# Kernel optimization log

Measured on AMD Instinct MI355X. Metric: run time of the kernel, lower is better.

The kernel has to match this reference:

```python
import jax, jax.numpy as jnp
import numpy as np

NUM_BITS = 10
MEM_SIZE = 2 ** NUM_BITS  # 1024
HIDDEN = 1024
INPUT = 1024
BATCH = 16384
LN_EPS = 1e-5


def setup_inputs() -> dict:
    key = jax.random.key(0)
    ks = jax.random.split(key, 8)
    s = 0.02
    return {
        "x": jax.random.normal(ks[0], (BATCH, INPUT), jnp.float32),
        "h_prev": jax.random.normal(ks[1], (BATCH, HIDDEN), jnp.float32),
        "memory": jax.random.normal(ks[2], (MEM_SIZE, HIDDEN), jnp.float32),
        "W_w": jax.random.normal(ks[3], (HIDDEN, INPUT), jnp.float32) * s,
        "W_b": jnp.zeros((HIDDEN,), jnp.float32),
        "U_w": jax.random.normal(ks[4], (HIDDEN, HIDDEN), jnp.float32) * s,
        "U_b": jnp.zeros((HIDDEN,), jnp.float32),
        "Q_w": jax.random.normal(ks[5], (HIDDEN, HIDDEN), jnp.float32) * s,
        "Q_b": jnp.zeros((HIDDEN,), jnp.float32),
        "M_w": jax.random.normal(ks[6], (NUM_BITS, HIDDEN), jnp.float32) * s,
        "M_b": jnp.zeros((NUM_BITS,), jnp.float32),
        "ln_g": jnp.ones((HIDDEN,), jnp.float32),
        "ln_b": jnp.zeros((HIDDEN,), jnp.float32),
    }


def reference(x, h_prev, memory, W_w, W_b, U_w, U_b, Q_w, Q_b, M_w, M_b, ln_g, ln_b):
    # Binary address from h_prev (eval-mode hard threshold, non-differentiable)
    powers = jnp.asarray(2 ** np.arange(NUM_BITS - 1, -1, -1), dtype=x.dtype)  # [num_bits]
    logits = h_prev @ M_w.T + M_b                              # [B, num_bits]
    binary = (jax.nn.sigmoid(logits) > 0.5).astype(x.dtype)    # hard bits
    index = jnp.clip((binary * powers).sum(-1).astype(jnp.int32), 0, MEM_SIZE - 1)  # [B]
    h_mem = memory[index]                                      # gather [B, H]
    # Fused linear combine + LayerNorm + sigmoid
    pre = x @ W_w.T + W_b + h_prev @ U_w.T + U_b + h_mem @ Q_w.T + Q_b  # [B, H]
    mu = pre.mean(-1, keepdims=True)
    var = ((pre - mu) ** 2).mean(-1, keepdims=True)            # biased var (torch LN)
    norm = (pre - mu) * jax.lax.rsqrt(var + LN_EPS)
    return jax.nn.sigmoid(norm * ln_g + ln_b)                  # h_new [B, H]
```

## Files before the change

### kernel.cpp

```cpp
#include <hip/hip_runtime.h>

#define BATCH   16384
#define HIDDEN  1024
#define K2      2048
#define MEMSZ   1024
#define NBITS   10

#define BM 256
#define BN 256
#define BK 64
#define NT (K2 / BK)

typedef __bf16 bf16x8 __attribute__((ext_vector_type(8)));
typedef float  f32x4  __attribute__((ext_vector_type(4)));

__device__ __forceinline__ unsigned short f2bf(float f) {
    unsigned int u = __float_as_uint(f);
    u += 0x7FFFu + ((u >> 16) & 1u);
    return (unsigned short)(u >> 16);
}

__device__ __forceinline__ void gload_lds16(const void* g, void* l) {
    __builtin_amdgcn_global_load_lds(
        (const __attribute__((address_space(1))) unsigned int*)g,
        (__attribute__((address_space(3))) unsigned int*)l,
        16, 0, 0);
}

__global__ void pack_kernel(const float* __restrict__ W,
                            const float* __restrict__ U,
                            const float* __restrict__ memory,
                            const float* __restrict__ Q,
                            unsigned short* __restrict__ Bm,
                            unsigned short* __restrict__ Mem,
                            unsigned short* __restrict__ Qb) {
    int u = blockIdx.x * 256 + threadIdx.x;
    const float* src;
    unsigned short* dst;
    if (u < 524288) {
        int n = u >> 9;
        int k = (u & 511) * 4;
        src = (k < 1024) ? (W + (size_t)n * 1024 + k)
                         : (U + (size_t)n * 1024 + (k - 1024));
        dst = Bm + (size_t)n * K2 + k;
    } else if (u < 786432) {
        int f = (u - 524288) * 4;
        src = memory + f;  dst = Mem + f;
    } else if (u < 1048576) {
        int f = (u - 786432) * 4;
        src = Q + f;  dst = Qb + f;
    } else return;
    float4 v = *reinterpret_cast<const float4*>(src);
    ushort4 o;
    o.x = f2bf(v.x); o.y = f2bf(v.y); o.z = f2bf(v.z); o.w = f2bf(v.w);
    *reinterpret_cast<ushort4*>(dst) = o;
}

__global__ __launch_bounds__(256) void mq_kernel(
        const unsigned short* __restrict__ Mem,
        const unsigned short* __restrict__ Qb,
        float* __restrict__ MQ) {
    __shared__ unsigned short As[128 * 64];
    __shared__ unsigned short Bs[128 * 64];

    const int ks = blockIdx.x >> 6;
    const int mb = (blockIdx.x >> 3) & 7;
    const int nb = blockIdx.x & 7;
    const int t    = threadIdx.x;
    const int lane = t & 63;
    const int w    = t >> 6;
    const int wr   = w >> 1, wc = w & 1;
    const int rr   = lane & 15, rq = lane >> 4;
    const int c8   = (t & 7) * 8;
    const int srow = t >> 3;

    f32x4 acc[4][4] = {};

    for (int kt = 0; kt < 4; ++kt) {
        const int k0 = ks * 256 + kt * 64;
#pragma unroll
        for (int i = 0; i < 4; ++i) {
            int r = i * 32 + srow;
            gload_lds16(Mem + (size_t)(mb * 128 + r) * 1024 + k0 + c8, As + i * 2048 + t * 8);
            gload_lds16(Qb  + (size_t)(nb * 128 + r) * 1024 + k0 + c8, Bs + i * 2048 + t * 8);
        }
        __syncthreads();
#pragma unroll
        for (int kk = 0; kk < 2; ++kk) {
            const int krd = kk * 32 + rq * 8;
            bf16x8 af[4], bfv[4];
#pragma unroll
            for (int m = 0; m < 4; ++m)
                af[m] = *reinterpret_cast<const bf16x8*>(As + (wr * 64 + m * 16 + rr) * 64 + krd);
#pragma unroll
            for (int n = 0; n < 4; ++n)
                bfv[n] = *reinterpret_cast<const bf16x8*>(Bs + (wc * 64 + n * 16 + rr) * 64 + krd);
#pragma unroll
            for (int m = 0; m < 4; ++m)
#pragma unroll
                for (int n = 0; n < 4; ++n)
                    acc[m][n] = __builtin_amdgcn_mfma_f32_16x16x32_bf16(
                        af[m], bfv[n], acc[m][n], 0, 0, 0);
        }
        __syncthreads();
    }

#pragma unroll
    for (int m = 0; m < 4; ++m)
#pragma unroll
        for (int n = 0; n < 4; ++n) {
            int gcol = nb * 128 + wc * 64 + n * 16 + rr;
#pragma unroll
            for (int j = 0; j < 4; ++j) {
                int grow = mb * 128 + wr * 64 + m * 16 + rq * 4 + j;
                atomicAdd(&MQ[(size_t)grow * 1024 + gcol], acc[m][n][j]);
            }
        }
}

__global__ __launch_bounds__(256) void build_a_kernel(
        const float* __restrict__ x,
        const float* __restrict__ h_prev,
        const float* __restrict__ M_w,
        const float* __restrict__ M_b,
        unsigned short* __restrict__ A,
        int* __restrict__ idxbuf) {
    int row  = (blockIdx.x * blockDim.x + threadIdx.x) >> 6;
    int lane = threadIdx.x & 63;
    if (row >= BATCH) return;

    const float4* hp = reinterpret_cast<const float4*>(h_prev + (size_t)row * HIDDEN);
    float4 hv[4];
#pragma unroll
    for (int i = 0; i < 4; ++i) hv[i] = hp[i * 64 + lane];

    int idx = 0;
#pragma unroll
    for (int j = 0; j < NBITS; ++j) {
        const float4* mp = reinterpret_cast<const float4*>(M_w + (size_t)j * HIDDEN);
        float s = 0.f;
#pragma unroll
        for (int i = 0; i < 4; ++i) {
            float4 m = mp[i * 64 + lane];
            s += hv[i].x * m.x + hv[i].y * m.y + hv[i].z * m.z + hv[i].w * m.w;
        }
#pragma unroll
        for (int off = 32; off >= 1; off >>= 1) s += __shfl_xor(s, off, 64);
        float logit = s + M_b[j];
        if (logit > 0.f) idx |= (1 << (NBITS - 1 - j));
    }
    if (lane == 0) idxbuf[row] = idx;

    unsigned short* arow = A + (size_t)row * K2;
    const float4* xp = reinterpret_cast<const float4*>(x + (size_t)row * HIDDEN);
#pragma unroll
    for (int i = 0; i < 4; ++i) {
        int off = i * 256 + lane * 4;
        float4 vx = xp[i * 64 + lane];
        ushort4 ox; ox.x = f2bf(vx.x); ox.y = f2bf(vx.y); ox.z = f2bf(vx.z); ox.w = f2bf(vx.w);
        *reinterpret_cast<ushort4*>(arow + off) = ox;

        ushort4 oh; oh.x = f2bf(hv[i].x); oh.y = f2bf(hv[i].y); oh.z = f2bf(hv[i].z); oh.w = f2bf(hv[i].w);
        *reinterpret_cast<ushort4*>(arow + 1024 + off) = oh;
    }
}


__device__ __forceinline__ void stage_g(const unsigned short* __restrict__ src,
                                        int rowbase, int kt, int g,
                                        unsigned short* ldsTile, int t) {
    const int o      = g * 8192 + t * 16;
    const int row    = o >> 7;
    const int inner  = o & 127;
    const int sinner = inner ^ ((row & 7) << 4);
    const char* gp = reinterpret_cast<const char*>(
                         src + (size_t)(rowbase + row) * K2 + kt * BK) + sinner;
    gload_lds16(gp, reinterpret_cast<char*>(ldsTile) + o);
}

__device__ __forceinline__ bf16x8 ldsfrag(const unsigned short* tile, int row,
                                          int kbyte_x_sw) {
    return *reinterpret_cast<const bf16x8*>(
        reinterpret_cast<const char*>(tile) + row * 128 + kbyte_x_sw);
}

#define BAR_IN()                                                     \
    do {                                                             \
        asm volatile("" ::: "memory");                               \
        __builtin_amdgcn_s_barrier();                                \
        asm volatile("s_waitcnt lgkmcnt(0)" ::: "memory");           \
        __builtin_amdgcn_sched_barrier(0);                           \
    } while (0)

#define BAR_OUT()                                                    \
    do {                                                             \
        __builtin_amdgcn_sched_barrier(0);                           \
        asm volatile("" ::: "memory");                               \
        __builtin_amdgcn_s_barrier();                                \
    } while (0)

#define MFMA_Q(MB, NB)                                                         \
    {                                                                          \
        __builtin_amdgcn_s_setprio(1);                                         \
        _Pragma("unroll") for (int m_ = 0; m_ < 4; ++m_)                       \
        _Pragma("unroll") for (int n_ = 0; n_ < 2; ++n_)                       \
        _Pragma("unroll") for (int kk_ = 0; kk_ < 2; ++kk_)                    \
            acc[(MB) + m_][(NB) + n_] =                                        \
                __builtin_amdgcn_mfma_f32_16x16x32_bf16(                       \
                    af[m_][kk_], bfr[(NB) + n_][kk_],                          \
                    acc[(MB) + m_][(NB) + n_], 0, 0, 0);                       \
        __builtin_amdgcn_s_setprio(0);                                         \
    }

__global__ __launch_bounds__(512, 2) void gemm_kernel(
        const unsigned short* __restrict__ A,
        const unsigned short* __restrict__ Bm,
        float* __restrict__ C) {
    __shared__ alignas(16) unsigned short lds[2][2][BM * BK];

    const int bid  = blockIdx.x;
    const int wgid = (bid & 7) * 32 + (bid >> 3);
    const int mblk = wgid >> 2;
    const int nblk = wgid & 3;

    const int t    = threadIdx.x;
    const int lane = t & 63;
    const int w    = t >> 6;
    const int wr   = w >> 2;
    const int wc   = w & 3;
    const int rr   = lane & 15;
    const int rq   = lane >> 4;
    const int sw   = (rr & 7) << 4;
    const int rqb  = rq * 16;
    const int wrb  = wr * 128;
    const int wcb  = wc * 64;

    const int arow = mblk * BM;
    const int brow = nblk * BN;

    f32x4 acc[8][4] = {};

    {
#pragma unroll
        for (int g = 0; g < 4; ++g) stage_g(A,  arow, 0, g, &lds[0][0][0], t);
#pragma unroll
        for (int g = 0; g < 4; ++g) stage_g(Bm, brow, 0, g, &lds[0][1][0], t);
#pragma unroll
        for (int g = 0; g < 4; ++g) stage_g(Bm, brow, 1, g, &lds[1][1][0], t);
#pragma unroll
        for (int g = 0; g < 2; ++g) stage_g(A,  arow, 1, g, &lds[1][0][0], t);
        asm volatile("s_waitcnt vmcnt(6)" ::: "memory");
        asm volatile("" ::: "memory");
        __builtin_amdgcn_s_barrier();
    }

    bf16x8 af[4][2];
    bf16x8 bfr[4][2];

#pragma unroll 2
    for (int kt = 0; kt < NT; ++kt) {
        const int c = kt & 1;
        const unsigned short* At = &lds[c][0][0];
        const unsigned short* Bt = &lds[c][1][0];
        unsigned short* nxA  = &lds[c ^ 1][0][0];
        unsigned short* curA = &lds[c][0][0];
        unsigned short* curB = &lds[c][1][0];

#pragma unroll
        for (int m = 0; m < 4; ++m) {
            af[m][0] = ldsfrag(At, wrb + m * 16 + rr, (rqb) ^ sw);
            af[m][1] = ldsfrag(At, wrb + m * 16 + rr, (64 + rqb) ^ sw);
        }
#pragma unroll
        for (int n = 0; n < 4; ++n) {
            bfr[n][0] = ldsfrag(Bt, wcb + n * 16 + rr, (rqb) ^ sw);
            bfr[n][1] = ldsfrag(Bt, wcb + n * 16 + rr, (64 + rqb) ^ sw);
        }
        if (kt + 1 < NT) {
            stage_g(A, arow, kt + 1, 2, nxA, t);
            stage_g(A, arow, kt + 1, 3, nxA, t);
        }
        BAR_IN();
        MFMA_Q(0, 0);
        BAR_OUT();

        BAR_IN();
        MFMA_Q(0, 2);
        BAR_OUT();

#pragma unroll
        for (int m = 0; m < 4; ++m) {
            af[m][0] = ldsfrag(At, wrb + 64 + m * 16 + rr, (rqb) ^ sw);
            af[m][1] = ldsfrag(At, wrb + 64 + m * 16 + rr, (64 + rqb) ^ sw);
        }
        if (kt + 2 < NT) {
            stage_g(Bm, brow, kt + 2, 0, curB, t);
            stage_g(Bm, brow, kt + 2, 1, curB, t);
        }
        BAR_IN();
        MFMA_Q(4, 0);
        BAR_OUT();

        if (kt + 2 < NT) {
            stage_g(Bm, brow, kt + 2, 2, curB, t);
            stage_g(Bm, brow, kt + 2, 3, curB, t);
            stage_g(A,  arow, kt + 2, 0, curA, t);
            stage_g(A,  arow, kt + 2, 1, curA, t);
        }
        BAR_IN();
        MFMA_Q(4, 2);
        __builtin_amdgcn_sched_barrier(0);
        if (kt < NT - 2) {
            asm volatile("s_waitcnt vmcnt(6)" ::: "memory");
        } else if (kt == NT - 2) {
            asm volatile("s_waitcnt vmcnt(0)" ::: "memory");
        }
        asm volatile("" ::: "memory");
        __builtin_amdgcn_s_barrier();
    }

#pragma unroll
    for (int mi = 0; mi < 8; ++mi) {
#pragma unroll
        for (int n = 0; n < 4; ++n) {
            const int gcol = nblk * BN + wcb + n * 16 + rr;
#pragma unroll
            for (int j = 0; j < 4; ++j) {
                const int grow = mblk * BM + wrb + mi * 16 + rq * 4 + j;
                C[(size_t)grow * HIDDEN + gcol] = acc[mi][n][j];
            }
        }
    }
}

__global__ __launch_bounds__(256) void ln_kernel(
        float* __restrict__ C,
        const int* __restrict__ idxbuf,
        const float* __restrict__ MQ,
        const float* __restrict__ W_b, const float* __restrict__ U_b,
        const float* __restrict__ Q_b, const float* __restrict__ ln_g,
        const float* __restrict__ ln_b) {
    const int row = blockIdx.x;
    const int t   = threadIdx.x;
    const int midx = idxbuf[row];
    float4* rowp = reinterpret_cast<float4*>(C + (size_t)row * HIDDEN);
    const float4* mqp = reinterpret_cast<const float4*>(MQ + (size_t)midx * HIDDEN);

    float4 p  = rowp[t];
    float4 mq = mqp[t];
    float4 bw = reinterpret_cast<const float4*>(W_b)[t];
    float4 bu = reinterpret_cast<const float4*>(U_b)[t];
    float4 bq = reinterpret_cast<const float4*>(Q_b)[t];
    p.x += mq.x + bw.x + bu.x + bq.x;
    p.y += mq.y + bw.y + bu.y + bq.y;
    p.z += mq.z + bw.z + bu.z + bq.z;
    p.w += mq.w + bw.w + bu.w + bq.w;

    float s  = p.x + p.y + p.z + p.w;
    float sq = p.x * p.x + p.y * p.y + p.z * p.z + p.w * p.w;
#pragma unroll
    for (int off = 32; off >= 1; off >>= 1) {
        s  += __shfl_xor(s,  off, 64);
        sq += __shfl_xor(sq, off, 64);
    }
    __shared__ float red[8];
    const int lane = t & 63, w = t >> 6;
    if (lane == 0) { red[w] = s; red[4 + w] = sq; }
    __syncthreads();
    const float S    = red[0] + red[1] + red[2] + red[3];
    const float SQ   = red[4] + red[5] + red[6] + red[7];
    const float mean = S * (1.0f / HIDDEN);
    const float var  = SQ * (1.0f / HIDDEN) - mean * mean;
    const float rstd = rsqrtf(var + 1e-5f);

    float4 g = reinterpret_cast<const float4*>(ln_g)[t];
    float4 b = reinterpret_cast<const float4*>(ln_b)[t];
    float4 o;
    o.x = 1.f / (1.f + __expf(-((p.x - mean) * rstd * g.x + b.x)));
    o.y = 1.f / (1.f + __expf(-((p.y - mean) * rstd * g.y + b.y)));
    o.z = 1.f / (1.f + __expf(-((p.z - mean) * rstd * g.z + b.z)));
    o.w = 1.f / (1.f + __expf(-((p.w - mean) * rstd * g.w + b.w)));
    rowp[t] = o;
}

extern "C" void kernel_launch(void* const* d_in, const int* in_sizes, int n_in,
                              void* d_out, int out_size, void* d_ws, size_t ws_size,
                              hipStream_t stream) {
    const float* x      = (const float*)d_in[0];
    const float* h_prev = (const float*)d_in[1];
    const float* memory = (const float*)d_in[2];
    const float* W_w    = (const float*)d_in[3];
    const float* W_b    = (const float*)d_in[4];
    const float* U_w    = (const float*)d_in[5];
    const float* U_b    = (const float*)d_in[6];
    const float* Q_w    = (const float*)d_in[7];
    const float* Q_b    = (const float*)d_in[8];
    const float* M_w    = (const float*)d_in[9];
    const float* M_b    = (const float*)d_in[10];
    const float* ln_g   = (const float*)d_in[11];
    const float* ln_b   = (const float*)d_in[12];

    char* ws = (char*)d_ws;
    unsigned short* A   = (unsigned short*)(ws);
    unsigned short* Bm  = (unsigned short*)(ws + 67108864);
    unsigned short* Mem = (unsigned short*)(ws + 71303168);
    unsigned short* Qb  = (unsigned short*)(ws + 73400320);
    float*          MQ  = (float*)         (ws + 75497472);
    int*            idx = (int*)           (ws + 79691776);
    float* pre = (float*)d_out;

    hipLaunchKernelGGL(pack_kernel, dim3(4096), dim3(256), 0, stream,
                       W_w, U_w, memory, Q_w, Bm, Mem, Qb);
    hipMemsetAsync(MQ, 0, (size_t)MEMSZ * HIDDEN * sizeof(float), stream);
    hipLaunchKernelGGL(mq_kernel, dim3(256), dim3(256), 0, stream,
                       Mem, Qb, MQ);
    hipLaunchKernelGGL(build_a_kernel, dim3(BATCH / 4), dim3(256), 0, stream,
                       x, h_prev, M_w, M_b, A, idx);
    hipLaunchKernelGGL(gemm_kernel, dim3((BATCH / BM) * (HIDDEN / BN)), dim3(512), 0, stream,
                       A, Bm, pre);
    hipLaunchKernelGGL(ln_kernel, dim3(BATCH), dim3(256), 0, stream,
                       pre, idx, MQ, W_b, U_b, Q_b, ln_g, ln_b);
}
```

Before: 173.2 us.

## Fuse fp32-to-bf16 A conversion into GEMM, dropping the packed A buffer

Stops materializing a packed bf16 A matrix (x and h_prev concatenated) in a separate kernel. The GEMM now loads fp32 x and h_prev into registers, converts them to bf16 and writes them into swizzled LDS, with the loads software-pipelined two k-tiles ahead. This removes a 64MB write and its later re-read, at the cost of twice the global bytes for A per GEMM tile (fp32, and re-read by the four N-blocks), more registers, and manual vmcnt accounting in place of direct-to-LDS loads.

```diff
diff --git a/kernel.cpp b/kernel.cpp
--- a/kernel.cpp
+++ b/kernel.cpp
@@ -118,12 +118,10 @@
         }
 }
 
-__global__ __launch_bounds__(256) void build_a_kernel(
-        const float* __restrict__ x,
+__global__ __launch_bounds__(256) void logits_kernel(
         const float* __restrict__ h_prev,
         const float* __restrict__ M_w,
         const float* __restrict__ M_b,
-        unsigned short* __restrict__ A,
         int* __restrict__ idxbuf) {
     int row  = (blockIdx.x * blockDim.x + threadIdx.x) >> 6;
     int lane = threadIdx.x & 63;
@@ -150,19 +148,6 @@
         if (logit > 0.f) idx |= (1 << (NBITS - 1 - j));
     }
     if (lane == 0) idxbuf[row] = idx;
-
-    unsigned short* arow = A + (size_t)row * K2;
-    const float4* xp = reinterpret_cast<const float4*>(x + (size_t)row * HIDDEN);
-#pragma unroll
-    for (int i = 0; i < 4; ++i) {
-        int off = i * 256 + lane * 4;
-        float4 vx = xp[i * 64 + lane];
-        ushort4 ox; ox.x = f2bf(vx.x); ox.y = f2bf(vx.y); ox.z = f2bf(vx.z); ox.w = f2bf(vx.w);
-        *reinterpret_cast<ushort4*>(arow + off) = ox;
-
-        ushort4 oh; oh.x = f2bf(hv[i].x); oh.y = f2bf(hv[i].y); oh.z = f2bf(hv[i].z); oh.w = f2bf(hv[i].w);
-        *reinterpret_cast<ushort4*>(arow + 1024 + off) = oh;
-    }
 }
 
 
@@ -176,6 +161,34 @@
     const char* gp = reinterpret_cast<const char*>(
                          src + (size_t)(rowbase + row) * K2 + kt * BK) + sinner;
     gload_lds16(gp, reinterpret_cast<char*>(ldsTile) + o);
+}
+
+__device__ __forceinline__ void loadA8(const float* __restrict__ base, int arow,
+                                       int kloc, int t, float4* va) {
+#pragma unroll
+    for (int g = 0; g < 4; ++g) {
+        const float* p = base + (size_t)(arow + g * 64 + (t >> 3)) * 1024
+                              + kloc + (t & 7) * 8;
+        va[2 * g]     = *reinterpret_cast<const float4*>(p);
+        va[2 * g + 1] = *reinterpret_cast<const float4*>(p + 4);
+    }
+}
+
+__device__ __forceinline__ void writeA(unsigned short* tile, int t,
+                                       const float4* va) {
+#pragma unroll
+    for (int g = 0; g < 4; ++g) {
+        bf16x8 v;
+#pragma unroll
+        for (int e = 0; e < 4; ++e) {
+            v[e]     = (__bf16)va[2 * g][e];
+            v[4 + e] = (__bf16)va[2 * g + 1][e];
+        }
+        const int o   = g * 8192 + t * 16;
+        const int row = o >> 7;
+        const int dst = (o & ~127) | ((o & 127) ^ ((row & 7) << 4));
+        *reinterpret_cast<bf16x8*>(reinterpret_cast<char*>(tile) + dst) = v;
+    }
 }
 
 __device__ __forceinline__ bf16x8 ldsfrag(const unsigned short* tile, int row,
@@ -213,7 +226,8 @@
     }
 
 __global__ __launch_bounds__(512, 2) void gemm_kernel(
-        const unsigned short* __restrict__ A,
+        const float* __restrict__ x,
+        const float* __restrict__ h_prev,
         const unsigned short* __restrict__ Bm,
         float* __restrict__ C) {
     __shared__ alignas(16) unsigned short lds[2][2][BM * BK];
@@ -239,18 +253,22 @@
     const int brow = nblk * BN;
 
     f32x4 acc[8][4] = {};
+    float4 va[8];
 
     {
-#pragma unroll
-        for (int g = 0; g < 4; ++g) stage_g(A,  arow, 0, g, &lds[0][0][0], t);
+        loadA8(x, arow, 0, t, va);
 #pragma unroll
         for (int g = 0; g < 4; ++g) stage_g(Bm, brow, 0, g, &lds[0][1][0], t);
+        asm volatile("s_waitcnt vmcnt(4)" ::: "memory");
+        writeA(&lds[0][0][0], t, va);
+
+        loadA8(x, arow, 64, t, va);
 #pragma unroll
         for (int g = 0; g < 4; ++g) stage_g(Bm, brow, 1, g, &lds[1][1][0], t);
-#pragma unroll
-        for (int g = 0; g < 2; ++g) stage_g(A,  arow, 1, g, &lds[1][0][0], t);
-        asm volatile("s_waitcnt vmcnt(6)" ::: "memory");
-        asm volatile("" ::: "memory");
+        asm volatile("s_waitcnt vmcnt(4)" ::: "memory");
+        writeA(&lds[1][0][0], t, va);
+
+        asm volatile("s_waitcnt lgkmcnt(0)" ::: "memory");
         __builtin_amdgcn_s_barrier();
     }
 
@@ -262,10 +280,14 @@
         const int c = kt & 1;
         const unsigned short* At = &lds[c][0][0];
         const unsigned short* Bt = &lds[c][1][0];
-        unsigned short* nxA  = &lds[c ^ 1][0][0];
         unsigned short* curA = &lds[c][0][0];
         unsigned short* curB = &lds[c][1][0];
-
+        const bool pf = (kt + 2 < NT);
+
+        if (pf) {
+            const float* abase = (kt + 2 < 16) ? x : h_prev;
+            loadA8(abase, arow, ((kt + 2) & 15) * 64, t, va);
+        }
 #pragma unroll
         for (int m = 0; m < 4; ++m) {
             af[m][0] = ldsfrag(At, wrb + m * 16 + rr, (rqb) ^ sw);
@@ -276,10 +298,6 @@
             bfr[n][0] = ldsfrag(Bt, wcb + n * 16 + rr, (rqb) ^ sw);
             bfr[n][1] = ldsfrag(Bt, wcb + n * 16 + rr, (64 + rqb) ^ sw);
         }
-        if (kt + 1 < NT) {
-            stage_g(A, arow, kt + 1, 2, nxA, t);
-            stage_g(A, arow, kt + 1, 3, nxA, t);
-        }
         BAR_IN();
         MFMA_Q(0, 0);
         BAR_OUT();
@@ -293,7 +311,7 @@
             af[m][0] = ldsfrag(At, wrb + 64 + m * 16 + rr, (rqb) ^ sw);
             af[m][1] = ldsfrag(At, wrb + 64 + m * 16 + rr, (64 + rqb) ^ sw);
         }
-        if (kt + 2 < NT) {
+        if (pf) {
             stage_g(Bm, brow, kt + 2, 0, curB, t);
             stage_g(Bm, brow, kt + 2, 1, curB, t);
         }
@@ -301,20 +319,17 @@
         MFMA_Q(4, 0);
         BAR_OUT();
 
-        if (kt + 2 < NT) {
+        if (pf) {
             stage_g(Bm, brow, kt + 2, 2, curB, t);
             stage_g(Bm, brow, kt + 2, 3, curB, t);
-            stage_g(A,  arow, kt + 2, 0, curA, t);
-            stage_g(A,  arow, kt + 2, 1, curA, t);
+            asm volatile("s_waitcnt vmcnt(4)" ::: "memory");
+            writeA(curA, t, va);
+        } else if (kt + 1 < NT) {
+            asm volatile("s_waitcnt vmcnt(0)" ::: "memory");
         }
         BAR_IN();
         MFMA_Q(4, 2);
         __builtin_amdgcn_sched_barrier(0);
-        if (kt < NT - 2) {
-            asm volatile("s_waitcnt vmcnt(6)" ::: "memory");
-        } else if (kt == NT - 2) {
-            asm volatile("s_waitcnt vmcnt(0)" ::: "memory");
-        }
         asm volatile("" ::: "memory");
         __builtin_amdgcn_s_barrier();
     }
@@ -401,12 +416,11 @@
     const float* ln_b   = (const float*)d_in[12];
 
     char* ws = (char*)d_ws;
-    unsigned short* A   = (unsigned short*)(ws);
-    unsigned short* Bm  = (unsigned short*)(ws + 67108864);
-    unsigned short* Mem = (unsigned short*)(ws + 71303168);
-    unsigned short* Qb  = (unsigned short*)(ws + 73400320);
-    float*          MQ  = (float*)         (ws + 75497472);
-    int*            idx = (int*)           (ws + 79691776);
+    unsigned short* Bm  = (unsigned short*)(ws);
+    unsigned short* Mem = (unsigned short*)(ws + 4194304);
+    unsigned short* Qb  = (unsigned short*)(ws + 6291456);
+    float*          MQ  = (float*)         (ws + 8388608);
+    int*            idx = (int*)           (ws + 12582912);
     float* pre = (float*)d_out;
 
     hipLaunchKernelGGL(pack_kernel, dim3(4096), dim3(256), 0, stream,
@@ -414,10 +428,10 @@
     hipMemsetAsync(MQ, 0, (size_t)MEMSZ * HIDDEN * sizeof(float), stream);
     hipLaunchKernelGGL(mq_kernel, dim3(256), dim3(256), 0, stream,
                        Mem, Qb, MQ);
-    hipLaunchKernelGGL(build_a_kernel, dim3(BATCH / 4), dim3(256), 0, stream,
-                       x, h_prev, M_w, M_b, A, idx);
+    hipLaunchKernelGGL(logits_kernel, dim3(BATCH / 4), dim3(256), 0, stream,
+                       h_prev, M_w, M_b, idx);
     hipLaunchKernelGGL(gemm_kernel, dim3((BATCH / BM) * (HIDDEN / BN)), dim3(512), 0, stream,
-                       A, Bm, pre);
+                       x, h_prev, Bm, pre);
     hipLaunchKernelGGL(ln_kernel, dim3(BATCH), dim3(256), 0, stream,
                        pre, idx, MQ, W_b, U_b, Q_b, ln_g, ln_b);
 }
```

After: 204.2 us. 1.18x slower.

## Software-pipeline LDS fragment loads across iterations with partial lgkmcnt waits

Applied to the files above, without the earlier changes.

Restructures the GEMM main loop so A/B fragments for the next k-tile are read from LDS during the current tile's last MFMA quadrant, using a second A fragment register set (af2). Full lgkmcnt(0) waits are replaced by graded partial waits, and the global prefetch stages and vmcnt thresholds are reordered. This overlaps LDS read latency with MFMA work, but adds register pressure under launch_bounds(512,2). The lgkmcnt counts and barrier placement become fragile, since a miscounted wait would read stale fragments.

```diff
diff --git a/kernel.cpp b/kernel.cpp
--- a/kernel.cpp
+++ b/kernel.cpp
@@ -184,11 +184,11 @@
         reinterpret_cast<const char*>(tile) + row * 128 + kbyte_x_sw);
 }
 
-#define BAR_IN()                                                     \
+#define WAIT_PH(N)                                                   \
     do {                                                             \
         asm volatile("" ::: "memory");                               \
         __builtin_amdgcn_s_barrier();                                \
-        asm volatile("s_waitcnt lgkmcnt(0)" ::: "memory");           \
+        asm volatile("s_waitcnt lgkmcnt(" #N ")" ::: "memory");      \
         __builtin_amdgcn_sched_barrier(0);                           \
     } while (0)
 
@@ -199,7 +199,7 @@
         __builtin_amdgcn_s_barrier();                                \
     } while (0)
 
-#define MFMA_Q(MB, NB)                                                         \
+#define MFMA_Q(AF, MB, NB)                                                     \
     {                                                                          \
         __builtin_amdgcn_s_setprio(1);                                         \
         _Pragma("unroll") for (int m_ = 0; m_ < 4; ++m_)                       \
@@ -207,7 +207,7 @@
         _Pragma("unroll") for (int kk_ = 0; kk_ < 2; ++kk_)                    \
             acc[(MB) + m_][(NB) + n_] =                                        \
                 __builtin_amdgcn_mfma_f32_16x16x32_bf16(                       \
-                    af[m_][kk_], bfr[(NB) + n_][kk_],                          \
+                    AF[m_][kk_], bfr[(NB) + n_][kk_],                          \
                     acc[(MB) + m_][(NB) + n_], 0, 0, 0);                       \
         __builtin_amdgcn_s_setprio(0);                                         \
     }
@@ -254,69 +254,90 @@
         __builtin_amdgcn_s_barrier();
     }
 
-    bf16x8 af[4][2];
+    bf16x8 af [4][2];
+    bf16x8 af2[4][2];
     bf16x8 bfr[4][2];
 
-#pragma unroll 2
+#pragma unroll
+    for (int m = 0; m < 4; ++m) {
+        af[m][0] = ldsfrag(&lds[0][0][0], wrb + m * 16 + rr, (rqb) ^ sw);
+        af[m][1] = ldsfrag(&lds[0][0][0], wrb + m * 16 + rr, (64 + rqb) ^ sw);
+    }
+#pragma unroll
+    for (int n = 0; n < 2; ++n) {
+        bfr[n][0] = ldsfrag(&lds[0][1][0], wcb + n * 16 + rr, (rqb) ^ sw);
+        bfr[n][1] = ldsfrag(&lds[0][1][0], wcb + n * 16 + rr, (64 + rqb) ^ sw);
+    }
+
     for (int kt = 0; kt < NT; ++kt) {
         const int c = kt & 1;
         const unsigned short* At = &lds[c][0][0];
         const unsigned short* Bt = &lds[c][1][0];
-        unsigned short* nxA  = &lds[c ^ 1][0][0];
+        const unsigned short* nxA = &lds[c ^ 1][0][0];
+        const unsigned short* nxB = &lds[c ^ 1][1][0];
         unsigned short* curA = &lds[c][0][0];
         unsigned short* curB = &lds[c][1][0];
-
-#pragma unroll
-        for (int m = 0; m < 4; ++m) {
-            af[m][0] = ldsfrag(At, wrb + m * 16 + rr, (rqb) ^ sw);
-            af[m][1] = ldsfrag(At, wrb + m * 16 + rr, (64 + rqb) ^ sw);
-        }
-#pragma unroll
-        for (int n = 0; n < 4; ++n) {
+        const bool pf1 = (kt + 1 < NT);
+        const bool pf2 = (kt + 2 < NT);
+
+#pragma unroll
+        for (int n = 2; n < 4; ++n) {
             bfr[n][0] = ldsfrag(Bt, wcb + n * 16 + rr, (rqb) ^ sw);
             bfr[n][1] = ldsfrag(Bt, wcb + n * 16 + rr, (64 + rqb) ^ sw);
         }
-        if (kt + 1 < NT) {
-            stage_g(A, arow, kt + 1, 2, nxA, t);
-            stage_g(A, arow, kt + 1, 3, nxA, t);
-        }
-        BAR_IN();
-        MFMA_Q(0, 0);
+        if (pf1) {
+            stage_g(A, arow, kt + 1, 2, (unsigned short*)nxA, t);
+            stage_g(A, arow, kt + 1, 3, (unsigned short*)nxA, t);
+        }
+        WAIT_PH(4);
+        MFMA_Q(af, 0, 0);
         BAR_OUT();
 
-        BAR_IN();
-        MFMA_Q(0, 2);
+#pragma unroll
+        for (int m = 0; m < 4; ++m) {
+            af2[m][0] = ldsfrag(At, wrb + 64 + m * 16 + rr, (rqb) ^ sw);
+            af2[m][1] = ldsfrag(At, wrb + 64 + m * 16 + rr, (64 + rqb) ^ sw);
+        }
+        WAIT_PH(8);
+        MFMA_Q(af, 0, 2);
         BAR_OUT();
 
-#pragma unroll
-        for (int m = 0; m < 4; ++m) {
-            af[m][0] = ldsfrag(At, wrb + 64 + m * 16 + rr, (rqb) ^ sw);
-            af[m][1] = ldsfrag(At, wrb + 64 + m * 16 + rr, (64 + rqb) ^ sw);
-        }
-        if (kt + 2 < NT) {
+        if (pf2) {
             stage_g(Bm, brow, kt + 2, 0, curB, t);
             stage_g(Bm, brow, kt + 2, 1, curB, t);
         }
-        BAR_IN();
-        MFMA_Q(4, 0);
-        BAR_OUT();
-
-        if (kt + 2 < NT) {
+        WAIT_PH(0);
+        MFMA_Q(af2, 4, 0);
+        __builtin_amdgcn_sched_barrier(0);
+        if (kt < NT - 2) {
+            asm volatile("s_waitcnt vmcnt(2)" ::: "memory");
+        } else if (kt == NT - 2) {
+            asm volatile("s_waitcnt vmcnt(0)" ::: "memory");
+        }
+        asm volatile("" ::: "memory");
+        __builtin_amdgcn_s_barrier();
+
+        if (pf1) {
+#pragma unroll
+            for (int m = 0; m < 4; ++m) {
+                af[m][0] = ldsfrag(nxA, wrb + m * 16 + rr, (rqb) ^ sw);
+                af[m][1] = ldsfrag(nxA, wrb + m * 16 + rr, (64 + rqb) ^ sw);
+            }
+#pragma unroll
+            for (int n = 0; n < 2; ++n) {
+                bfr[n][0] = ldsfrag(nxB, wcb + n * 16 + rr, (rqb) ^ sw);
+                bfr[n][1] = ldsfrag(nxB, wcb + n * 16 + rr, (64 + rqb) ^ sw);
+            }
+        }
+        if (pf2) {
             stage_g(Bm, brow, kt + 2, 2, curB, t);
             stage_g(Bm, brow, kt + 2, 3, curB, t);
             stage_g(A,  arow, kt + 2, 0, curA, t);
             stage_g(A,  arow, kt + 2, 1, curA, t);
         }
-        BAR_IN();
-        MFMA_Q(4, 2);
-        __builtin_amdgcn_sched_barrier(0);
-        if (kt < NT - 2) {
-            asm volatile("s_waitcnt vmcnt(6)" ::: "memory");
-        } else if (kt == NT - 2) {
-            asm volatile("s_waitcnt vmcnt(0)" ::: "memory");
-        }
-        asm volatile("" ::: "memory");
-        __builtin_amdgcn_s_barrier();
+        if (pf1) { WAIT_PH(12); } else { WAIT_PH(0); }
+        MFMA_Q(af2, 4, 2);
+        BAR_OUT();
     }
 
 #pragma unroll
```

After: 170.2 us. About the same (-1.7%).
